# Optimization experiments

Hardware: AMD Instinct MI355X
Metric: run time of the kernel (lower is better)

Reference implementation:

```python
import jax, jax.numpy as jnp
import numpy as np

D_MODEL = 1024
D_STATE = 16
D_CONV = 4
EXPAND = 2
D_INNER = D_MODEL * EXPAND
B_SZ = 2
SEQ = 4096


def setup_inputs() -> dict:
    key = jax.random.key(0)
    ks = jax.random.split(key, 11)
    rn = lambda i, shape, scale=1.0: jax.random.normal(ks[i], shape, jnp.float32) * scale
    return {
        "x": rn(0, (B_SZ, SEQ, D_MODEL)),
        "W_in": rn(1, (D_MODEL, D_INNER), D_MODEL ** -0.5),
        "b_in": rn(2, (D_INNER,), 0.01),
        "conv_w": rn(3, (D_INNER, 1, D_CONV), 0.1),   # torch depthwise layout [out_ch, in_ch/groups=1, k]
        "conv_b": rn(4, (D_INNER,), 0.01),
        # A scaled so tanh(A) is contractive -> stable recurrence over 4096 steps
        "A": rn(5, (D_STATE, D_STATE), 0.1),
        "Bp": rn(6, (D_STATE,)),   # B parameter [d_state, 1] flattened
        "Cp": rn(7, (D_STATE,)),   # C parameter [1, d_state] flattened
        "Dp": rn(8, (1,)),
        "W_out": rn(9, (D_INNER, D_MODEL), D_INNER ** -0.5),
        "b_out": rn(10, (D_MODEL,), 0.01),
    }


def reference(x, W_in, b_in, conv_w, conv_b, A, Bp, Cp, Dp, W_out, b_out):
    Bsz, S, _ = x.shape
    d_inner = W_in.shape[1]
    # input projection
    u = x @ W_in + b_in                              # [B, S, d_inner]
    # causal depthwise conv (torch pads k-1 both sides then slices [:S])
    u = u.transpose(0, 2, 1)                         # [B, d_inner, S]
    u = jax.lax.conv_general_dilated(
        u, conv_w, window_strides=(1,), padding=[(D_CONV - 1, 0)],
        dimension_numbers=("NCH", "OIH", "NCH"),
        feature_group_count=d_inner) + conv_b[None, :, None]
    u = u.transpose(0, 2, 1)                         # [B, S, d_inner]
    # per-channel scalar SSM shared across channels: h_t = tanh(A) h_{t-1} + B u_t; y_t = C h_t + D u_t
    At = jnp.tanh(A)                                 # [ds, ds]
    def step(h, u_t):                                # h: [B, d_inner, ds], u_t: [B, d_inner]
        h = jnp.einsum("ij,bdj->bdi", At, h) + u_t[..., None] * Bp
        y = jnp.einsum("j,bdj->bd", Cp, h) + Dp[0] * u_t
        return h, y
    h0 = jnp.zeros((Bsz, d_inner, Bp.shape[0]), x.dtype)
    _, ys = jax.lax.scan(step, h0, u.transpose(1, 0, 2))  # ys: [S, B, d_inner]
    y = jax.nn.silu(ys.transpose(1, 0, 2))           # [B, S, d_inner]
    return y @ W_out + b_out                         # [B, S, d_model]
```

## Files before the change

kernel.cpp:

```cpp
#include <hip/hip_runtime.h>

typedef unsigned short u16;
typedef float  f32x4  __attribute__((ext_vector_type(4)));
typedef __bf16 bf16x8 __attribute__((ext_vector_type(8)));
typedef u16    u16x2  __attribute__((ext_vector_type(2)));
typedef u16    u16x4  __attribute__((ext_vector_type(4)));

#define D_MODEL 1024
#define D_INNER 2048
#define B_SZ    2
#define SEQ     4096
#define MROWS   (B_SZ * SEQ)
#define LTAPS   64
#define VROW    136

__device__ __forceinline__ u16 f2bf(float f) {
    return __builtin_bit_cast(u16, (__bf16)f);
}
__device__ __forceinline__ float bf2f(u16 h) {
    unsigned u = ((unsigned)h) << 16;
    return __builtin_bit_cast(float, u);
}

typedef __attribute__((address_space(1))) void gv_t;
typedef __attribute__((address_space(3))) void lv_t;
__device__ __forceinline__ void glds16(const u16* g, u16* l) {
    __builtin_amdgcn_global_load_lds((gv_t*)g, (lv_t*)l, 16, 0, 0);
}
#define WAIT_VM(n) (0x0F70 | (n))
#define WAIT_LGKM0 0xC07F

__device__ __forceinline__ void transpose_tile(
    const float* __restrict__ in, u16* __restrict__ out,
    int R, int C, int c0, int r0, int tid, float (*tile)[33])
{
    const int tx = tid & 31, ty = tid >> 5;
    for (int k = 0; k < 32; k += 8)
        tile[ty + k][tx] = in[(size_t)(r0 + ty + k) * C + c0 + tx];
    __syncthreads();
    for (int k = 0; k < 32; k += 8)
        out[(size_t)(c0 + ty + k) * R + r0 + tx] = f2bf(tile[tx][ty + k]);
}

__global__ __launch_bounds__(256) void prep_kernel(
    const float* __restrict__ x, u16* __restrict__ xb,
    const float* __restrict__ Win, u16* __restrict__ WinT,
    const float* __restrict__ Wout, u16* __restrict__ WoutT,
    const float* __restrict__ A, const float* __restrict__ Bp,
    const float* __restrict__ Cp, const float* __restrict__ Dp,
    u16* __restrict__ Amat64)
{
    __shared__ float tile[32][33];
    __shared__ float fs[LTAPS];
    const int bx = blockIdx.x, tid = threadIdx.x;
    if (bx < 8192) {
        size_t i = ((size_t)bx * 256 + tid) * 4;
        f32x4 v = *(const f32x4*)(x + i);
        u16x4 o;
        o.x = f2bf(v.x); o.y = f2bf(v.y); o.z = f2bf(v.z); o.w = f2bf(v.w);
        *(u16x4*)(xb + i) = o;
    } else if (bx < 10240) {
        const int flat = bx - 8192;
        transpose_tile(Win, WinT, 1024, 2048,
                       (flat & 63) * 32, (flat >> 6) * 32, tid, tile);
    } else if (bx < 12288) {
        const int flat = bx - 10240;
        transpose_tile(Wout, WoutT, 2048, 1024,
                       (flat & 31) * 32, (flat >> 5) * 32, tid, tile);
    } else {
        if (tid < 64) {
            const int i = tid & 15;
            float Atr[16];
            for (int j = 0; j < 16; j++) Atr[j] = tanhf(A[i * 16 + j]);
            float p = Bp[i];
            const float c  = Cp[i];
            const float d0 = Dp[0];
            for (int t = 0; t < LTAPS; t++) {
                float fv = c * p;
                fv += __shfl_xor(fv, 1); fv += __shfl_xor(fv, 2);
                fv += __shfl_xor(fv, 4); fv += __shfl_xor(fv, 8);
                if (tid == 0) fs[t] = fv + (t == 0 ? d0 : 0.f);
                float n0 = 0.f, n1 = 0.f, n2 = 0.f, n3 = 0.f;
                #pragma unroll
                for (int j = 0; j < 4; j++) {
                    n0 = fmaf(Atr[j],      __shfl(p, j),      n0);
                    n1 = fmaf(Atr[j + 4],  __shfl(p, j + 4),  n1);
                    n2 = fmaf(Atr[j + 8],  __shfl(p, j + 8),  n2);
                    n3 = fmaf(Atr[j + 12], __shfl(p, j + 12), n3);
                }
                p = (n0 + n1) + (n2 + n3);
            }
        }
        __syncthreads();
        for (int idx = tid; idx < 64 * 128; idx += 256) {
            const int i = idx >> 7, j = idx & 127;
            const int tau = 64 + i - j;
            float v = (tau >= 0 && tau < LTAPS) ? fs[tau] : 0.f;
            Amat64[idx] = f2bf(v);
        }
    }
}

template <int MODE>
__global__ __launch_bounds__(512, 2) void gemm_p4_kernel(
    const u16* __restrict__ A, const u16* __restrict__ BT,
    void* __restrict__ Cout, const float* __restrict__ bias,
    int N, int K)
{
    constexpr int REGU = (256 + 128) * 32;
    __shared__ __align__(16) u16 sm[4 * REGU];
    const int tid = threadIdx.x, lane = tid & 63;
    const int wid = tid >> 6;
    const int bid = blockIdx.x;
    const int xcd = bid & 7, loc = bid >> 3;
    const int mt = xcd * 4 + (loc & 3), nt = loc >> 2;
    const int m0 = mt * 256, n0 = nt * 128;
    const int wm = wid & 3, wn = wid >> 2;
    const int fr = lane & 15, fq = lane >> 4;

    auto mk = [&](const u16* G, int r0, int q) -> const u16* {
        const int l = q ^ (((q >> 7) & 7) << 4);
        return G + (size_t)(r0 + (l >> 6)) * K + ((l & 63) >> 1);
    };
    const u16* pA0 = mk(A, m0, tid * 16);
    const u16* pA1 = mk(A, m0, tid * 16 + 8192);
    const u16* pB0 = mk(BT, n0, tid * 16);

    auto glds_half = [&](int p) {
        u16* rb = sm + (p & 3) * REGU;
        const int ko = p * 32;
        glds16(pA0 + ko, rb + tid * 8);
        glds16(pA1 + ko, rb + tid * 8 + 4096);
        glds16(pB0 + ko, rb + 8192 + tid * 8);
    };

    int aoff[4], boff[4];
    #pragma unroll
    for (int i = 0; i < 4; ++i) {
        const int la = (wm * 64 + i * 16 + fr) * 64 + fq * 16;
        aoff[i] = (la ^ (((la >> 7) & 7) << 4)) >> 1;
        const int lb = (wn * 64 + i * 16 + fr) * 64 + fq * 16;
        boff[i] = ((lb ^ (((lb >> 7) & 7) << 4)) >> 1) + 8192;
    }

    f32x4 acc[4][4] = {};
    const int NPH = K >> 5;

    glds_half(0); glds_half(1); glds_half(2);
    asm volatile("" ::: "memory");
    __builtin_amdgcn_s_waitcnt(WAIT_VM(6));
    __builtin_amdgcn_sched_barrier(0);
    __builtin_amdgcn_s_barrier();

#define P4_PHASE(p, ISSUE, WVM, LAST)                                        \
  {                                                                          \
    const u16* rb_ = sm + ((p) & 3) * REGU;                                  \
    bf16x8 af[4], bfr[4];                                                    \
    _Pragma("unroll")                                                        \
    for (int i = 0; i < 4; ++i) af[i]  = *(const bf16x8*)(rb_ + aoff[i]);    \
    _Pragma("unroll")                                                        \
    for (int i = 0; i < 4; ++i) bfr[i] = *(const bf16x8*)(rb_ + boff[i]);    \
    if (ISSUE) glds_half((p) + 3);                                           \
    asm volatile("" ::: "memory");                                           \
    __builtin_amdgcn_sched_barrier(0);                                       \
    __builtin_amdgcn_s_barrier();                                            \
    __builtin_amdgcn_s_waitcnt(WAIT_LGKM0);                                  \
    __builtin_amdgcn_sched_barrier(0);                                       \
    __builtin_amdgcn_s_setprio(1);                                           \
    _Pragma("unroll")                                                        \
    for (int mi = 0; mi < 4; ++mi)                                           \
      _Pragma("unroll")                                                      \
      for (int ni = 0; ni < 4; ++ni)                                         \
        acc[mi][ni] = __builtin_amdgcn_mfma_f32_16x16x32_bf16(               \
            bfr[ni], af[mi], acc[mi][ni], 0, 0, 0);                          \
    __builtin_amdgcn_s_setprio(0);                                           \
    if (!(LAST)) {                                                           \
      asm volatile("" ::: "memory");                                         \
      __builtin_amdgcn_s_waitcnt(WAIT_VM(WVM));                              \
      __builtin_amdgcn_sched_barrier(0);                                     \
      __builtin_amdgcn_s_barrier();                                          \
    }                                                                        \
  }

    #pragma unroll 1
    for (int p = 0; p < NPH - 3; ++p)
        P4_PHASE(p, true, 6, false)
    P4_PHASE(NPH - 3, false, 3, false)
    P4_PHASE(NPH - 2, false, 0, false)
    P4_PHASE(NPH - 1, false, 0, true)
#undef P4_PHASE

    #pragma unroll
    for (int ni = 0; ni < 4; ++ni) {
        const int colb = n0 + wn * 64 + ni * 16 + fq * 4;
        const f32x4 bv = *(const f32x4*)(bias + colb);
        #pragma unroll
        for (int mi = 0; mi < 4; ++mi) {
            const int row = m0 + wm * 64 + mi * 16 + fr;
            f32x4 v = acc[mi][ni];
            v.x += bv.x; v.y += bv.y; v.z += bv.z; v.w += bv.w;
            if constexpr (MODE == 0) {
                u16x4 o;
                o.x = f2bf(v.x); o.y = f2bf(v.y); o.z = f2bf(v.z); o.w = f2bf(v.w);
                *(u16x4*)((u16*)Cout + (size_t)row * N + colb) = o;
            } else {
                *(f32x4*)((float*)Cout + (size_t)row * N + colb) = v;
            }
        }
    }
}

__global__ __launch_bounds__(256) void conv_fir_mfma_kernel(
    const u16* __restrict__ u, const float* __restrict__ cw,
    const float* __restrict__ cb, const u16* __restrict__ Amat64,
    u16* __restrict__ Y)
{
    __shared__ u16 VT[128 * VROW];
    const int tid = threadIdx.x;
    const int c0 = blockIdx.x * 128, t0 = blockIdx.y * 64, b = blockIdx.z;
    {
        const int tx = tid & 63, ty = tid >> 6;
        const int cg = c0 + tx * 2;
        const f32x4 wA = *(const f32x4*)(cw + cg * 4);
        const f32x4 wB = *(const f32x4*)(cw + cg * 4 + 4);
        const float cb0 = cb[cg], cb1 = cb[cg + 1];
        const u16* ucol = u + (size_t)b * SEQ * D_INNER + cg;
        const int s0 = t0 - 64 + ty * 32;
        u16* vr0 = VT + (tx * 2)     * VROW + ty * 32;
        u16* vr1 = VT + (tx * 2 + 1) * VROW + ty * 32;
        if (t0 == 0 && ty < 2) {
            const u16x4 z = {0, 0, 0, 0};
            #pragma unroll
            for (int j = 0; j < 8; j++) {
                *(u16x4*)(vr0 + j * 4) = z;
                *(u16x4*)(vr1 + j * 4) = z;
            }
        } else {
            float am3 = 0.f, am2 = 0.f, am1 = 0.f;
            float bm3 = 0.f, bm2 = 0.f, bm1 = 0.f;
            if (s0 > 0) {
                u16x2 d3 = *(const u16x2*)(ucol + (size_t)(s0 - 3) * D_INNER);
                u16x2 d2 = *(const u16x2*)(ucol + (size_t)(s0 - 2) * D_INNER);
                u16x2 d1 = *(const u16x2*)(ucol + (size_t)(s0 - 1) * D_INNER);
                am3 = bf2f(d3.x); bm3 = bf2f(d3.y);
                am2 = bf2f(d2.x); bm2 = bf2f(d2.y);
                am1 = bf2f(d1.x); bm1 = bf2f(d1.y);
            }
            #pragma unroll 2
            for (int j = 0; j < 8; j++) {
                const u16* p = ucol + (size_t)(s0 + j * 4) * D_INNER;
                u16x2 r0 = *(const u16x2*)(p);
                u16x2 r1 = *(const u16x2*)(p + (size_t)D_INNER);
                u16x2 r2 = *(const u16x2*)(p + (size_t)2 * D_INNER);
                u16x2 r3 = *(const u16x2*)(p + (size_t)3 * D_INNER);
                float a0 = bf2f(r0.x), b0 = bf2f(r0.y);
                float a1 = bf2f(r1.x), b1 = bf2f(r1.y);
                float a2 = bf2f(r2.x), b2 = bf2f(r2.y);
                float a3 = bf2f(r3.x), b3 = bf2f(r3.y);
                u16x4 oa, ob;
                oa.x = f2bf(cb0 + wA.x * am3 + wA.y * am2 + wA.z * am1 + wA.w * a0);
                oa.y = f2bf(cb0 + wA.x * am2 + wA.y * am1 + wA.z * a0  + wA.w * a1);
                oa.z = f2bf(cb0 + wA.x * am1 + wA.y * a0  + wA.z * a1  + wA.w * a2);
                oa.w = f2bf(cb0 + wA.x * a0  + wA.y * a1  + wA.z * a2  + wA.w * a3);
                ob.x = f2bf(cb1 + wB.x * bm3 + wB.y * bm2 + wB.z * bm1 + wB.w * b0);
                ob.y = f2bf(cb1 + wB.x * bm2 + wB.y * bm1 + wB.z * b0  + wB.w * b1);
                ob.z = f2bf(cb1 + wB.x * bm1 + wB.y * b0  + wB.z * b1  + wB.w * b2);
                ob.w = f2bf(cb1 + wB.x * b0  + wB.y * b1  + wB.z * b2  + wB.w * b3);
                *(u16x4*)(vr0 + j * 4) = oa;
                *(u16x4*)(vr1 + j * 4) = ob;
                am3 = a1; am2 = a2; am1 = a3;
                bm3 = b1; bm2 = b2; bm1 = b3;
            }
        }
    }
    __syncthreads();
    const int lane = tid & 63, wid = tid >> 6;
    const int wm = (wid & 1) * 32, wn = (wid >> 1) * 64;
    const int fr = lane & 15, fq = lane >> 4;
    f32x4 acc[2][4] = {};
    #pragma unroll
    for (int kq = 0; kq < 4; kq++) {
        const int k0 = kq * 32;
        bf16x8 af[2], bfr[4];
        #pragma unroll
        for (int mi = 0; mi < 2; mi++)
            af[mi] = *(const bf16x8*)(Amat64 + (wm + mi * 16 + fr) * 128 + k0 + fq * 8);
        #pragma unroll
        for (int ni = 0; ni < 4; ni++)
            bfr[ni] = *(const bf16x8*)(VT + (wn + ni * 16 + fr) * VROW + k0 + fq * 8);
        #pragma unroll
        for (int mi = 0; mi < 2; mi++)
            #pragma unroll
            for (int ni = 0; ni < 4; ni++)
                acc[mi][ni] = __builtin_amdgcn_mfma_f32_16x16x32_bf16(
                    bfr[ni], af[mi], acc[mi][ni], 0, 0, 0);
    }
    #pragma unroll
    for (int ni = 0; ni < 4; ni++) {
        const int cbase = c0 + wn + ni * 16 + fq * 4;
        #pragma unroll
        for (int mi = 0; mi < 2; mi++) {
            const int trow = t0 + wm + mi * 16 + fr;
            f32x4 v = acc[mi][ni];
            u16x4 o;
            o.x = f2bf(v.x / (1.f + __expf(-v.x)));
            o.y = f2bf(v.y / (1.f + __expf(-v.y)));
            o.z = f2bf(v.z / (1.f + __expf(-v.z)));
            o.w = f2bf(v.w / (1.f + __expf(-v.w)));
            *(u16x4*)(Y + ((size_t)(b * SEQ + trow)) * D_INNER + cbase) = o;
        }
    }
}

extern "C" void kernel_launch(void* const* d_in, const int* in_sizes, int n_in,
                              void* d_out, int out_size, void* d_ws, size_t ws_size,
                              hipStream_t stream)
{
    const float* x    = (const float*)d_in[0];
    const float* Win  = (const float*)d_in[1];
    const float* bin  = (const float*)d_in[2];
    const float* cw   = (const float*)d_in[3];
    const float* cb   = (const float*)d_in[4];
    const float* A    = (const float*)d_in[5];
    const float* Bp   = (const float*)d_in[6];
    const float* Cp   = (const float*)d_in[7];
    const float* Dp   = (const float*)d_in[8];
    const float* Wout = (const float*)d_in[9];
    const float* bout = (const float*)d_in[10];
    float* out = (float*)d_out;

    char* ws = (char*)d_ws;
    u16* xb     = (u16*)(ws);
    u16* WinT   = (u16*)(ws + 16777216);
    u16* WoutT  = (u16*)(ws + 20971520);
    u16* u      = (u16*)(ws + 25165824);
    u16* Y      = (u16*)(ws + 58720256);
    u16* Amat64 = (u16*)(ws + 92274688);

    prep_kernel<<<12289, 256, 0, stream>>>(x, xb, Win, WinT, Wout, WoutT,
                                           A, Bp, Cp, Dp, Amat64);
    gemm_p4_kernel<0><<<512, 512, 0, stream>>>(xb, WinT, u, bin,
                                               D_INNER, D_MODEL);
    conv_fir_mfma_kernel<<<dim3(16, 64, 2), 256, 0, stream>>>(u, cw, cb, Amat64, Y);
    gemm_p4_kernel<1><<<256, 512, 0, stream>>>(Y, WoutT, out, bout,
                                               D_MODEL, D_INNER);
}
```

Baseline: 247.7 us.

## Enlarge GEMM tiles to 256x256 and split-K the output projection with atomics

```diff
diff --git a/kernel.cpp b/kernel.cpp
--- a/kernel.cpp
+++ b/kernel.cpp
@@ -27,7 +27,8 @@
 __device__ __forceinline__ void glds16(const u16* g, u16* l) {
     __builtin_amdgcn_global_load_lds((gv_t*)g, (lv_t*)l, 16, 0, 0);
 }
-#define WAIT_VM(n) (0x0F70 | (n))
+#define WAIT_VM4   0x0F74
+#define WAIT_VM0   0x0F70
 #define WAIT_LGKM0 0xC07F
 
 __device__ __forceinline__ void transpose_tile(
@@ -48,7 +49,8 @@
     const float* __restrict__ Wout, u16* __restrict__ WoutT,
     const float* __restrict__ A, const float* __restrict__ Bp,
     const float* __restrict__ Cp, const float* __restrict__ Dp,
-    u16* __restrict__ Amat64)
+    u16* __restrict__ Amat64,
+    const float* __restrict__ bout, float* __restrict__ outp)
 {
     __shared__ float tile[32][33];
     __shared__ float fs[LTAPS];
@@ -67,7 +69,7 @@
         const int flat = bx - 10240;
         transpose_tile(Wout, WoutT, 2048, 1024,
                        (flat & 31) * 32, (flat >> 5) * 32, tid, tile);
-    } else {
+    } else if (bx == 12288) {
         if (tid < 64) {
             const int i = tid & 15;
             float Atr[16];
@@ -98,69 +100,89 @@
             float v = (tau >= 0 && tau < LTAPS) ? fs[tau] : 0.f;
             Amat64[idx] = f2bf(v);
         }
+    } else {
+        const size_t e = ((size_t)(bx - 12289) * 256 + tid) * 4;
+        const int col = (int)(e & 1023);
+        *(f32x4*)(outp + e) = *(const f32x4*)(bout + col);
     }
 }
 
 template <int MODE>
-__global__ __launch_bounds__(512, 2) void gemm_p4_kernel(
-    const u16* __restrict__ A, const u16* __restrict__ BT,
+__global__ __launch_bounds__(512, 2) void gemm_r4_kernel(
+    const u16* __restrict__ Ain, const u16* __restrict__ BT,
     void* __restrict__ Cout, const float* __restrict__ bias,
-    int N, int K)
-{
-    constexpr int REGU = (256 + 128) * 32;
-    __shared__ __align__(16) u16 sm[4 * REGU];
-    const int tid = threadIdx.x, lane = tid & 63;
-    const int wid = tid >> 6;
+    int N, int Kst, int Klen)
+{
+    constexpr int BUFU = 16384;
+    __shared__ __align__(16) u16 sm[4 * BUFU];
+    const int tid = threadIdx.x, lane = tid & 63, wid = tid >> 6;
     const int bid = blockIdx.x;
     const int xcd = bid & 7, loc = bid >> 3;
-    const int mt = xcd * 4 + (loc & 3), nt = loc >> 2;
-    const int m0 = mt * 256, n0 = nt * 128;
-    const int wm = wid & 3, wn = wid >> 2;
+    const int mt = xcd * 4 + (loc & 3);
+    const int rest = loc >> 2;
+    int nt, ks;
+    if constexpr (MODE == 0) { nt = rest;     ks = 0; }
+    else                     { nt = rest & 3; ks = rest >> 2; }
+    const int m0 = mt * 256, n0 = nt * 256;
+    const int wm = wid & 1, wn = wid >> 1;
     const int fr = lane & 15, fq = lane >> 4;
+
+    const u16* Aeff = Ain + (size_t)ks * Klen;
+    const u16* Beff = BT  + (size_t)ks * Klen;
 
     auto mk = [&](const u16* G, int r0, int q) -> const u16* {
         const int l = q ^ (((q >> 7) & 7) << 4);
-        return G + (size_t)(r0 + (l >> 6)) * K + ((l & 63) >> 1);
+        return G + (size_t)(r0 + (l >> 6)) * Kst + ((l & 63) >> 1);
     };
-    const u16* pA0 = mk(A, m0, tid * 16);
-    const u16* pA1 = mk(A, m0, tid * 16 + 8192);
-    const u16* pB0 = mk(BT, n0, tid * 16);
-
-    auto glds_half = [&](int p) {
-        u16* rb = sm + (p & 3) * REGU;
-        const int ko = p * 32;
-        glds16(pA0 + ko, rb + tid * 8);
-        glds16(pA1 + ko, rb + tid * 8 + 4096);
-        glds16(pB0 + ko, rb + 8192 + tid * 8);
+    const u16* pA0 = mk(Aeff, m0, tid * 16);
+    const u16* pA1 = mk(Aeff, m0, tid * 16 + 8192);
+    const u16* pB0 = mk(Beff, n0, tid * 16);
+    const u16* pB1 = mk(Beff, n0, tid * 16 + 8192);
+
+    auto stageA = [&](int t) {
+        u16* bb = sm + (t & 3) * BUFU + (wid << 9);
+        glds16(pA0 + t * 32, bb);
+        glds16(pA1 + t * 32, bb + 4096);
     };
-
-    int aoff[4], boff[4];
-    #pragma unroll
-    for (int i = 0; i < 4; ++i) {
-        const int la = (wm * 64 + i * 16 + fr) * 64 + fq * 16;
-        aoff[i] = (la ^ (((la >> 7) & 7) << 4)) >> 1;
-        const int lb = (wn * 64 + i * 16 + fr) * 64 + fq * 16;
-        boff[i] = ((lb ^ (((lb >> 7) & 7) << 4)) >> 1) + 8192;
-    }
-
-    f32x4 acc[4][4] = {};
-    const int NPH = K >> 5;
-
-    glds_half(0); glds_half(1); glds_half(2);
+    auto stageB = [&](int t) {
+        u16* bb = sm + (t & 3) * BUFU + 8192 + (wid << 9);
+        glds16(pB0 + t * 32, bb);
+        glds16(pB1 + t * 32, bb + 4096);
+    };
+
+    int aoff[2][4], boff[4];
+    #pragma unroll
+    for (int rh = 0; rh < 2; ++rh)
+        #pragma unroll
+        for (int mi = 0; mi < 4; ++mi) {
+            const int la = (wm * 128 + rh * 64 + mi * 16 + fr) * 64 + fq * 16;
+            aoff[rh][mi] = (la ^ (((la >> 7) & 7) << 4)) >> 1;
+        }
+    #pragma unroll
+    for (int ni = 0; ni < 4; ++ni) {
+        const int lb = (wn * 64 + ni * 16 + fr) * 64 + fq * 16;
+        boff[ni] = ((lb ^ (((lb >> 7) & 7) << 4)) >> 1) + 8192;
+    }
+
+    f32x4 acc[8][4] = {};
+    bf16x8 af[4], bfr[4];
+    const int NT = Klen >> 5;
+
+    stageA(0); stageB(0); stageA(1); stageB(1);
     asm volatile("" ::: "memory");
-    __builtin_amdgcn_s_waitcnt(WAIT_VM(6));
+    __builtin_amdgcn_s_waitcnt(WAIT_VM4);
     __builtin_amdgcn_sched_barrier(0);
     __builtin_amdgcn_s_barrier();
 
-#define P4_PHASE(p, ISSUE, WVM, LAST)                                        \
+#define R4_TILE(t, STAGE, WVM, LAST)                                         \
   {                                                                          \
-    const u16* rb_ = sm + ((p) & 3) * REGU;                                  \
-    bf16x8 af[4], bfr[4];                                                    \
-    _Pragma("unroll")                                                        \
-    for (int i = 0; i < 4; ++i) af[i]  = *(const bf16x8*)(rb_ + aoff[i]);    \
-    _Pragma("unroll")                                                        \
-    for (int i = 0; i < 4; ++i) bfr[i] = *(const bf16x8*)(rb_ + boff[i]);    \
-    if (ISSUE) glds_half((p) + 3);                                           \
+    const u16* cb_ = sm + ((t) & 3) * BUFU;                                  \
+             \
+    _Pragma("unroll")                                                        \
+    for (int i = 0; i < 4; ++i) af[i]  = *(const bf16x8*)(cb_ + aoff[0][i]); \
+    _Pragma("unroll")                                                        \
+    for (int i = 0; i < 4; ++i) bfr[i] = *(const bf16x8*)(cb_ + boff[i]);    \
+    if (STAGE) stageA((t) + 2);                                              \
     asm volatile("" ::: "memory");                                           \
     __builtin_amdgcn_sched_barrier(0);                                       \
     __builtin_amdgcn_s_barrier();                                            \
@@ -174,37 +196,58 @@
         acc[mi][ni] = __builtin_amdgcn_mfma_f32_16x16x32_bf16(               \
             bfr[ni], af[mi], acc[mi][ni], 0, 0, 0);                          \
     __builtin_amdgcn_s_setprio(0);                                           \
+    asm volatile("" ::: "memory");                                           \
+    __builtin_amdgcn_s_barrier();                                            \
+         \
+    _Pragma("unroll")                                                        \
+    for (int i = 0; i < 4; ++i) af[i] = *(const bf16x8*)(cb_ + aoff[1][i]);  \
+    if (STAGE) stageB((t) + 2);                                              \
+    asm volatile("" ::: "memory");                                           \
+    if ((WVM) >= 0) __builtin_amdgcn_s_waitcnt((WVM) ? WAIT_VM4 : WAIT_VM0); \
+    __builtin_amdgcn_sched_barrier(0);                                       \
+    __builtin_amdgcn_s_barrier();                                            \
+    __builtin_amdgcn_s_waitcnt(WAIT_LGKM0);                                  \
+    __builtin_amdgcn_sched_barrier(0);                                       \
+    __builtin_amdgcn_s_setprio(1);                                           \
+    _Pragma("unroll")                                                        \
+    for (int mi = 0; mi < 4; ++mi)                                           \
+      _Pragma("unroll")                                                      \
+      for (int ni = 0; ni < 4; ++ni)                                         \
+        acc[4 + mi][ni] = __builtin_amdgcn_mfma_f32_16x16x32_bf16(           \
+            bfr[ni], af[mi], acc[4 + mi][ni], 0, 0, 0);                      \
+    __builtin_amdgcn_s_setprio(0);                                           \
     if (!(LAST)) {                                                           \
       asm volatile("" ::: "memory");                                         \
-      __builtin_amdgcn_s_waitcnt(WAIT_VM(WVM));                              \
-      __builtin_amdgcn_sched_barrier(0);                                     \
       __builtin_amdgcn_s_barrier();                                          \
     }                                                                        \
   }
 
     #pragma unroll 1
-    for (int p = 0; p < NPH - 3; ++p)
-        P4_PHASE(p, true, 6, false)
-    P4_PHASE(NPH - 3, false, 3, false)
-    P4_PHASE(NPH - 2, false, 0, false)
-    P4_PHASE(NPH - 1, false, 0, true)
-#undef P4_PHASE
+    for (int t = 0; t < NT - 2; ++t)
+        R4_TILE(t, true, 1, false)
+    R4_TILE(NT - 2, false, 0, false)
+    R4_TILE(NT - 1, false, -1, true)
+#undef R4_TILE
 
     #pragma unroll
     for (int ni = 0; ni < 4; ++ni) {
         const int colb = n0 + wn * 64 + ni * 16 + fq * 4;
-        const f32x4 bv = *(const f32x4*)(bias + colb);
-        #pragma unroll
-        for (int mi = 0; mi < 4; ++mi) {
-            const int row = m0 + wm * 64 + mi * 16 + fr;
+        #pragma unroll
+        for (int mi = 0; mi < 8; ++mi) {
+            const int row = m0 + wm * 128 + mi * 16 + fr;
             f32x4 v = acc[mi][ni];
-            v.x += bv.x; v.y += bv.y; v.z += bv.z; v.w += bv.w;
             if constexpr (MODE == 0) {
+                const f32x4 bv = *(const f32x4*)(bias + colb);
+                v.x += bv.x; v.y += bv.y; v.z += bv.z; v.w += bv.w;
                 u16x4 o;
                 o.x = f2bf(v.x); o.y = f2bf(v.y); o.z = f2bf(v.z); o.w = f2bf(v.w);
                 *(u16x4*)((u16*)Cout + (size_t)row * N + colb) = o;
             } else {
-                *(f32x4*)((float*)Cout + (size_t)row * N + colb) = v;
+                float* po = (float*)Cout + (size_t)row * N + colb;
+                __hip_atomic_fetch_add(po + 0, v.x, __ATOMIC_RELAXED, __HIP_MEMORY_SCOPE_AGENT);
+                __hip_atomic_fetch_add(po + 1, v.y, __ATOMIC_RELAXED, __HIP_MEMORY_SCOPE_AGENT);
+                __hip_atomic_fetch_add(po + 2, v.z, __ATOMIC_RELAXED, __HIP_MEMORY_SCOPE_AGENT);
+                __hip_atomic_fetch_add(po + 3, v.w, __ATOMIC_RELAXED, __HIP_MEMORY_SCOPE_AGENT);
             }
         }
     }
@@ -337,11 +380,11 @@
     u16* Y      = (u16*)(ws + 58720256);
     u16* Amat64 = (u16*)(ws + 92274688);
 
-    prep_kernel<<<12289, 256, 0, stream>>>(x, xb, Win, WinT, Wout, WoutT,
-                                           A, Bp, Cp, Dp, Amat64);
-    gemm_p4_kernel<0><<<512, 512, 0, stream>>>(xb, WinT, u, bin,
-                                               D_INNER, D_MODEL);
+    prep_kernel<<<20481, 256, 0, stream>>>(x, xb, Win, WinT, Wout, WoutT,
+                                           A, Bp, Cp, Dp, Amat64, bout, out);
+    gemm_r4_kernel<0><<<256, 512, 0, stream>>>(xb, WinT, u, bin,
+                                               D_INNER, D_MODEL, D_MODEL);
     conv_fir_mfma_kernel<<<dim3(16, 64, 2), 256, 0, stream>>>(u, cw, cb, Amat64, Y);
-    gemm_p4_kernel<1><<<256, 512, 0, stream>>>(Y, WoutT, out, bout,
-                                               D_MODEL, D_INNER);
-}
+    gemm_r4_kernel<2><<<256, 512, 0, stream>>>(Y, WoutT, out, nullptr,
+                                               D_MODEL, D_INNER, D_MODEL);
+}
```

Result: slower. 420.0 us (+69.5%).
